# Kernel tuning notes

Hardware: AMD Instinct MI355X
Metric: run time of the kernel (lower is better)

The kernel has to match this reference:

```python
import jax, jax.numpy as jnp
import numpy as np

B, L, DK, DV, H = 2, 2048, 512, 512, 8
DH_K = DK // H  # 64
DH_V = DV // H  # 64


def setup_inputs() -> dict:
    key = jax.random.key(0)
    ks = jax.random.split(key, 6)
    scale_w = 1.0 / np.sqrt(DK)
    return {
        "keys": jax.random.normal(ks[0], (B, L, DK), dtype=jnp.float32),
        "queries": jax.random.normal(ks[1], (B, L, DK), dtype=jnp.float32),
        "values": jax.random.normal(ks[2], (B, L, DV), dtype=jnp.float32),
        "WQ": jax.random.normal(ks[3], (H, DK, DH_K), dtype=jnp.float32) * scale_w,
        "WK": jax.random.normal(ks[4], (H, DK, DH_K), dtype=jnp.float32) * scale_w,
        "WV": jax.random.normal(ks[5], (H, DV, DH_V), dtype=jnp.float32) * scale_w,
    }


def reference(keys, queries, values, WQ, WK, WV):
    # Per-head projections, vectorized over all H heads at once.
    Q = jnp.einsum('bld,hde->bhle', queries, WQ)   # [B,H,Lq,dh]
    K = jnp.einsum('bld,hde->bhle', keys, WK)      # [B,H,Lk,dh]
    V = jnp.einsum('bld,hde->bhle', values, WV)    # [B,H,Lk,dv_h]
    Lk = keys.shape[1]
    # NOTE: original scales by sqrt(seq_len_k), not sqrt(head_dim).
    y = jnp.einsum('bhqe,bhke->bhqk', Q, K) / jnp.sqrt(jnp.float32(Lk))
    # NOTE: original applies softmax over torch dim=1 of [B,Lq,Lk],
    # i.e. the QUERY axis (axis=2 here in [B,H,Lq,Lk]).
    z = jax.nn.softmax(y, axis=2)
    out = jnp.einsum('bhqk,bhke->bhqe', z, V)      # [B,H,Lq,dv_h]
    # Concat heads on the feature dim (same order as torch.concat(..., 2)).
    Bq, Hh, Lq, Dh = out.shape
    return out.transpose(0, 2, 1, 3).reshape(Bq, Lq, Hh * Dh)
```

## Files before the change

kernel.cpp:

```cpp
#include <hip/hip_runtime.h>
#include <hip/hip_bf16.h>

#define LL 2048
#define DM 512
#define SCALE 0.02209708691207961f

typedef unsigned short u16;
typedef __attribute__((ext_vector_type(8))) short short8;
typedef __attribute__((ext_vector_type(4))) short short4v;
typedef __attribute__((ext_vector_type(4))) float f32x4;

#define XAQ_OFF 0u
#define XAK_OFF 2097152u
#define WB_OFF  4194304u
#define QB_OFF  4980736u
#define KB_OFF  7077888u
#define VT_OFF  9175040u
#define SV_OFF  11272192u

__device__ __forceinline__ u16 f2bf(float f) {
  union { float f; unsigned u; } v; v.f = f;
  unsigned r = v.u + 0x7fff + ((v.u >> 16) & 1);
  return (u16)(r >> 16);
}
__device__ __forceinline__ float bf2f(u16 u) {
  union { unsigned u; float f; } v; v.u = ((unsigned)u) << 16; return v.f;
}

__global__ __launch_bounds__(256) void prep_kernel(
    const float* __restrict__ queries, const float* __restrict__ keys,
    const float* __restrict__ WQ, const float* __restrict__ WK,
    const float* __restrict__ WV, u16* __restrict__ wsb) {
  int t = threadIdx.x;
  if (blockIdx.x < 2048) {
    size_t c = (size_t)blockIdx.x * 256 + t;
    int tens = (int)(c >> 18);
    size_t off = (c & 262143u) * 8;
    int b  = (int)(off >> 20);
    int l  = (int)((off >> 9) & 2047);
    int d8 = (int)((off & 511) >> 3);
    int kt = d8 >> 2, quad = d8 & 3;
    const float* src = (tens ? keys : queries) + off;
    float4 a = *(const float4*)(src);
    float4 bb = *(const float4*)(src + 4);
    short8 o;
    o[0] = (short)f2bf(a.x); o[1] = (short)f2bf(a.y);
    o[2] = (short)f2bf(a.z); o[3] = (short)f2bf(a.w);
    o[4] = (short)f2bf(bb.x); o[5] = (short)f2bf(bb.y);
    o[6] = (short)f2bf(bb.z); o[7] = (short)f2bf(bb.w);
    size_t dst = (tens ? XAK_OFF : XAQ_OFF) +
        ((((size_t)b * 128 + (l >> 4)) * 16 + kt) * 64 + (quad * 16 + (l & 15))) * 8;
    *(short8*)(wsb + dst) = o;
  } else {
    int c2 = (blockIdx.x - 2048) * 256 + t;
    int lane = c2 & 63;
    int nt = (c2 >> 6) & 3;
    int kt = (c2 >> 8) & 15;
    int h  = (c2 >> 12) & 7;
    int z  = c2 >> 15;
    int quad = lane >> 4, l16 = lane & 15;
    const float* W = (z == 0) ? WQ : (z == 1) ? WK : WV;
    const float* src = W + ((size_t)h * DM + kt * 32 + quad * 8) * 64 + nt * 16 + l16;
    short8 o;
#pragma unroll
    for (int j = 0; j < 8; ++j) o[j] = (short)f2bf(src[(size_t)j * 64]);
    *(short8*)(wsb + WB_OFF + (size_t)c2 * 8) = o;
  }
}

__global__ __launch_bounds__(256) void proj_kernel(const float* __restrict__ values,
                                                   u16* __restrict__ wsb) {
  int t = threadIdx.x;
  int lane = t & 63, w = t >> 6, quad = lane >> 4, l16 = lane & 15;
  int z = blockIdx.z, bh = blockIdx.y, b = bh >> 3, h = bh & 7;
  int qbase = blockIdx.x * 64;

  const u16* Bw = wsb + WB_OFF + ((size_t)(z * 8 + h) * 16) * 4 * 64 * 8;

  __shared__ __align__(16) short As[64 * 40];

  f32x4 acc[4];
#pragma unroll
  for (int nt = 0; nt < 4; ++nt) acc[nt] = (f32x4){0.f, 0.f, 0.f, 0.f};

  if (z < 2) {
    const u16* Ab = wsb + ((z == 0) ? XAQ_OFF : XAK_OFF) +
        (((size_t)b * 128 + (qbase >> 4) + w) * 16) * 64 * 8;
#pragma unroll 4
    for (int kt = 0; kt < 16; ++kt) {
      short8 a = *(const short8*)(Ab + ((size_t)kt * 64 + lane) * 8);
#pragma unroll
      for (int nt = 0; nt < 4; ++nt) {
        short8 bb = *(const short8*)(Bw + (((size_t)kt * 4 + nt) * 64 + lane) * 8);
        acc[nt] = __builtin_amdgcn_mfma_f32_16x16x32_bf16(a, bb, acc[nt], 0, 0, 0);
      }
    }
  } else {
    const float* inbase = values + ((size_t)b * LL + qbase) * DM;
    for (int kt = 0; kt < 16; ++kt) {
      __syncthreads();
#pragma unroll
      for (int rep = 0; rep < 2; ++rep) {
        int f4 = t + rep * 256;
        int row = f4 >> 3, c4 = f4 & 7;
        float4 v = *(const float4*)(inbase + (size_t)row * DM + kt * 32 + c4 * 4);
        short* dst = &As[row * 40 + c4 * 4];
        dst[0] = (short)f2bf(v.x); dst[1] = (short)f2bf(v.y);
        dst[2] = (short)f2bf(v.z); dst[3] = (short)f2bf(v.w);
      }
      __syncthreads();
      short8 a = *(const short8*)&As[(w * 16 + l16) * 40 + quad * 8];
#pragma unroll
      for (int nt = 0; nt < 4; ++nt) {
        short8 bb = *(const short8*)(Bw + (((size_t)kt * 4 + nt) * 64 + lane) * 8);
        acc[nt] = __builtin_amdgcn_mfma_f32_16x16x32_bf16(a, bb, acc[nt], 0, 0, 0);
      }
    }
  }

  if (z == 0) {
    u16* og = wsb + QB_OFF + ((size_t)bh * LL + qbase) * 64;
#pragma unroll
    for (int nt = 0; nt < 4; ++nt)
#pragma unroll
      for (int r = 0; r < 4; ++r)
        og[(size_t)(w * 16 + quad * 4 + r) * 64 + nt * 16 + l16] = f2bf(acc[nt][r] * SCALE);
  } else if (z == 1) {
    u16* og = wsb + KB_OFF + ((size_t)bh * LL + qbase) * 64;
#pragma unroll
    for (int nt = 0; nt < 4; ++nt)
#pragma unroll
      for (int r = 0; r < 4; ++r)
        og[(size_t)(w * 16 + quad * 4 + r) * 64 + nt * 16 + l16] = f2bf(acc[nt][r]);
  } else {
    u16* og = wsb + VT_OFF + (size_t)bh * 64 * LL;
#pragma unroll
    for (int nt = 0; nt < 4; ++nt)
#pragma unroll
      for (int r = 0; r < 4; ++r)
        og[(size_t)(nt * 16 + l16) * LL + qbase + w * 16 + quad * 4 + r] = f2bf(acc[nt][r]);
  }
}

__global__ __launch_bounds__(256) void stats_kernel(u16* __restrict__ wsb,
                                                    float* __restrict__ Sinv) {
  const u16* Qb = wsb + QB_OFF;
  const u16* Kb = wsb + KB_OFF;
  int t = threadIdx.x;
  int lane = t & 63, w = t >> 6, quad = lane >> 4, l16 = lane & 15;
  int bh = blockIdx.y;
  int kbase = blockIdx.x * 64;

  short8 ka0 = *(const short8*)(Kb + ((size_t)bh * LL + kbase + w * 16 + l16) * 64 + quad * 8);
  short8 ka1 = *(const short8*)(Kb + ((size_t)bh * LL + kbase + w * 16 + l16) * 64 + quad * 8 + 32);

  __shared__ __align__(16) u16 Qsh[64 * 72];
  __shared__ float Ss[64];

  int srow = t >> 3, sc8 = t & 7;
  int srow2 = (t + 256) >> 3;

  const u16* Qg = Qb + (size_t)bh * LL * 64;
  short8 rq0 = *(const short8*)(Qg + (size_t)srow * 64 + sc8 * 8);
  short8 rq1 = *(const short8*)(Qg + (size_t)srow2 * 64 + sc8 * 8);

  float rs[4] = {0.f, 0.f, 0.f, 0.f};
  for (int qt = 0; qt < 32; ++qt) {
    __syncthreads();
    *(short8*)&Qsh[srow * 72 + sc8 * 8] = rq0;
    *(short8*)&Qsh[srow2 * 72 + sc8 * 8] = rq1;
    rq0 = *(const short8*)(Qg + (size_t)((qt + 1) * 64 + srow) * 64 + sc8 * 8);
    rq1 = *(const short8*)(Qg + (size_t)((qt + 1) * 64 + srow2) * 64 + sc8 * 8);
    __syncthreads();
#pragma unroll
    for (int nt = 0; nt < 4; ++nt) {
      short8 b0 = *(const short8*)&Qsh[(nt * 16 + l16) * 72 + quad * 8];
      short8 b1 = *(const short8*)&Qsh[(nt * 16 + l16) * 72 + quad * 8 + 32];
      f32x4 y = (f32x4){0.f, 0.f, 0.f, 0.f};
      y = __builtin_amdgcn_mfma_f32_16x16x32_bf16(ka0, b0, y, 0, 0, 0);
      y = __builtin_amdgcn_mfma_f32_16x16x32_bf16(ka1, b1, y, 0, 0, 0);
#pragma unroll
      for (int r = 0; r < 4; ++r) rs[r] += __expf(y[r]);
    }
  }
#pragma unroll
  for (int r = 0; r < 4; ++r) {
    rs[r] += __shfl_xor(rs[r], 1);
    rs[r] += __shfl_xor(rs[r], 2);
    rs[r] += __shfl_xor(rs[r], 4);
    rs[r] += __shfl_xor(rs[r], 8);
  }
  if (l16 == 0) {
#pragma unroll
    for (int r = 0; r < 4; ++r) {
      float s = 1.0f / rs[r];
      Sinv[(size_t)bh * LL + kbase + w * 16 + quad * 4 + r] = s;
      Ss[w * 16 + quad * 4 + r] = s;
    }
  }
  __syncthreads();
#pragma unroll
  for (int rep = 0; rep < 2; ++rep) {
    int f8 = t + rep * 256;
    int e = f8 >> 3, c8 = f8 & 7;
    size_t ad = VT_OFF + ((size_t)bh * 64 + e) * LL + kbase + c8 * 8;
    short8 v = *(const short8*)(wsb + ad);
#pragma unroll
    for (int i = 0; i < 8; ++i)
      v[i] = (short)f2bf(bf2f((u16)v[i]) * Ss[c8 * 8 + i]);
    *(short8*)(wsb + ad) = v;
  }
}

__global__ __launch_bounds__(256) void attn_kernel(const u16* __restrict__ wsb,
                                                   float* __restrict__ out) {
  const u16* Qb = wsb + QB_OFF;
  const u16* Kb = wsb + KB_OFF;
  const u16* Vt = wsb + VT_OFF;
  int t = threadIdx.x;
  int lane = t & 63, w = t >> 6, quad = lane >> 4, l16 = lane & 15;
  int bh = blockIdx.y, b = bh >> 3, h = bh & 7;
  int qbase = blockIdx.x * 64;

  __shared__ __align__(16) u16 Ksh[64 * 72];
  __shared__ __align__(16) u16 Vsh[64 * 72];
  __shared__ __align__(16) u16 Ps[4 * 16 * 72];
  u16* psw = Ps + w * 16 * 72;

  short8 qa0 = *(const short8*)(Qb + ((size_t)bh * LL + qbase + w * 16 + l16) * 64 + quad * 8);
  short8 qa1 = *(const short8*)(Qb + ((size_t)bh * LL + qbase + w * 16 + l16) * 64 + quad * 8 + 32);

  int srow = t >> 3, sc8 = t & 7;
  int srow2 = (t + 256) >> 3;
  const u16* Kg = Kb + (size_t)bh * LL * 64;
  const u16* Vg = Vt + (size_t)bh * 64 * LL;

  short8 rk0 = *(const short8*)(Kg + (size_t)srow * 64 + sc8 * 8);
  short8 rk1 = *(const short8*)(Kg + (size_t)srow2 * 64 + sc8 * 8);
  short8 rv0 = *(const short8*)(Vg + (size_t)srow * LL + sc8 * 8);
  short8 rv1 = *(const short8*)(Vg + (size_t)srow2 * LL + sc8 * 8);

  f32x4 oacc[4];
#pragma unroll
  for (int nt = 0; nt < 4; ++nt) oacc[nt] = (f32x4){0.f, 0.f, 0.f, 0.f};

  for (int kt = 0; kt < 32; ++kt) {
    __syncthreads();
    *(short8*)&Ksh[srow * 72 + sc8 * 8] = rk0;
    *(short8*)&Ksh[srow2 * 72 + sc8 * 8] = rk1;
    *(short8*)&Vsh[srow * 72 + sc8 * 8] = rv0;
    *(short8*)&Vsh[srow2 * 72 + sc8 * 8] = rv1;
    rk0 = *(const short8*)(Kg + (size_t)((kt + 1) * 64 + srow) * 64 + sc8 * 8);
    rk1 = *(const short8*)(Kg + (size_t)((kt + 1) * 64 + srow2) * 64 + sc8 * 8);
    rv0 = *(const short8*)(Vg + (size_t)srow * LL + (kt + 1) * 64 + sc8 * 8);
    rv1 = *(const short8*)(Vg + (size_t)srow2 * LL + (kt + 1) * 64 + sc8 * 8);
    __syncthreads();

#pragma unroll
    for (int mt = 0; mt < 4; ++mt) {
      short8 a0 = *(const short8*)&Ksh[(mt * 16 + l16) * 72 + quad * 8];
      short8 a1 = *(const short8*)&Ksh[(mt * 16 + l16) * 72 + quad * 8 + 32];
      f32x4 y = (f32x4){0.f, 0.f, 0.f, 0.f};
      y = __builtin_amdgcn_mfma_f32_16x16x32_bf16(a0, qa0, y, 0, 0, 0);
      y = __builtin_amdgcn_mfma_f32_16x16x32_bf16(a1, qa1, y, 0, 0, 0);
      short4v p;
      p[0] = (short)f2bf(__expf(y[0]));
      p[1] = (short)f2bf(__expf(y[1]));
      p[2] = (short)f2bf(__expf(y[2]));
      p[3] = (short)f2bf(__expf(y[3]));
      *(short4v*)&psw[l16 * 72 + mt * 16 + quad * 4] = p;
    }
    short8 pa0 = *(const short8*)&psw[l16 * 72 + quad * 8];
    short8 pa1 = *(const short8*)&psw[l16 * 72 + quad * 8 + 32];
#pragma unroll
    for (int nt = 0; nt < 4; ++nt) {
      short8 v0 = *(const short8*)&Vsh[(nt * 16 + l16) * 72 + quad * 8];
      short8 v1 = *(const short8*)&Vsh[(nt * 16 + l16) * 72 + quad * 8 + 32];
      oacc[nt] = __builtin_amdgcn_mfma_f32_16x16x32_bf16(pa0, v0, oacc[nt], 0, 0, 0);
      oacc[nt] = __builtin_amdgcn_mfma_f32_16x16x32_bf16(pa1, v1, oacc[nt], 0, 0, 0);
    }
  }

  float* og = out + ((size_t)b * LL + qbase) * 512 + h * 64;
#pragma unroll
  for (int nt = 0; nt < 4; ++nt)
#pragma unroll
    for (int r = 0; r < 4; ++r)
      og[(size_t)(w * 16 + quad * 4 + r) * 512 + nt * 16 + l16] = oacc[nt][r];
}

extern "C" void kernel_launch(void* const* d_in, const int* in_sizes, int n_in,
                              void* d_out, int out_size, void* d_ws, size_t ws_size,
                              hipStream_t stream) {
  const float* keys    = (const float*)d_in[0];
  const float* queries = (const float*)d_in[1];
  const float* values  = (const float*)d_in[2];
  const float* WQ      = (const float*)d_in[3];
  const float* WK      = (const float*)d_in[4];
  const float* WV      = (const float*)d_in[5];
  float* out = (float*)d_out;
  u16* wsb = (u16*)d_ws;
  float* Sinv = (float*)(wsb + SV_OFF);

  prep_kernel<<<dim3(2048 + 384), 256, 0, stream>>>(queries, keys, WQ, WK, WV, wsb);
  proj_kernel<<<dim3(32, 16, 3), 256, 0, stream>>>(values, wsb);
  stats_kernel<<<dim3(32, 16), 256, 0, stream>>>(wsb, Sinv);
  attn_kernel<<<dim3(32, 16), 256, 0, stream>>>(wsb, out);
}
```

Baseline: 157.3 us.

## Store Q/K/V in MFMA fragment order and drop LDS staging in attention

The projection now writes Q and K directly in MFMA operand-fragment order. The stats kernel writes scaled V in a fragment layout suited to the 16x16x16 MFMA. The attention kernel loads operands straight from global memory without LDS tiles or barriers in the main loop. Each wave handles a slice of the key dimension for all 64 queries, and the partial outputs are reduced through shared memory at the end. This removes per-iteration syncthreads and the LDS round-trip for P, but adds more accumulator registers (launch bounds of 2), a large LDS reduction buffer and an extra final reduction.

New measurement: 147.5 us. 1.07x faster.

```diff
diff --git a/kernel.cpp b/kernel.cpp
--- a/kernel.cpp
+++ b/kernel.cpp
@@ -13,10 +13,10 @@
 #define XAQ_OFF 0u
 #define XAK_OFF 2097152u
 #define WB_OFF  4194304u
-#define QB_OFF  4980736u
-#define KB_OFF  7077888u
+#define QA_OFF  4980736u
+#define KA_OFF  7077888u
 #define VT_OFF  9175040u
-#define SV_OFF  11272192u
+#define VB_OFF  11272192u
 
 __device__ __forceinline__ u16 f2bf(float f) {
   union { float f; unsigned u; } v; v.f = f;
@@ -25,6 +25,12 @@
 }
 __device__ __forceinline__ float bf2f(u16 u) {
   union { unsigned u; float f; } v; v.u = ((unsigned)u) << 16; return v.f;
+}
+__device__ __forceinline__ size_t frag_idx(int bh, int t64, int w, int c, int lane) {
+  return ((((size_t)(bh * 32 + t64) * 4 + w) * 2 + c) * 64 + lane) * 8;
+}
+__device__ __forceinline__ size_t vb_idx(int bh, int kt, int w, int et, int lane) {
+  return ((((size_t)(bh * 32 + kt) * 4 + w) * 4 + et) * 64 + lane) * 4;
 }
 
 __global__ __launch_bounds__(256) void prep_kernel(
@@ -73,10 +79,9 @@
   int t = threadIdx.x;
   int lane = t & 63, w = t >> 6, quad = lane >> 4, l16 = lane & 15;
   int z = blockIdx.z, bh = blockIdx.y, b = bh >> 3, h = bh & 7;
-  int qbase = blockIdx.x * 64;
+  int QT = blockIdx.x, qbase = QT * 64;
 
   const u16* Bw = wsb + WB_OFF + ((size_t)(z * 8 + h) * 16) * 4 * 64 * 8;
-
   __shared__ __align__(16) short As[64 * 40];
 
   f32x4 acc[4];
@@ -118,20 +123,20 @@
     }
   }
 
-  if (z == 0) {
-    u16* og = wsb + QB_OFF + ((size_t)bh * LL + qbase) * 64;
-#pragma unroll
-    for (int nt = 0; nt < 4; ++nt)
-#pragma unroll
-      for (int r = 0; r < 4; ++r)
-        og[(size_t)(w * 16 + quad * 4 + r) * 64 + nt * 16 + l16] = f2bf(acc[nt][r] * SCALE);
-  } else if (z == 1) {
-    u16* og = wsb + KB_OFF + ((size_t)bh * LL + qbase) * 64;
-#pragma unroll
-    for (int nt = 0; nt < 4; ++nt)
-#pragma unroll
-      for (int r = 0; r < 4; ++r)
-        og[(size_t)(w * 16 + quad * 4 + r) * 64 + nt * 16 + l16] = f2bf(acc[nt][r]);
+  if (z < 2) {
+    u16* base = wsb + ((z == 0) ? QA_OFF : KA_OFF);
+    float sc = (z == 0) ? SCALE : 1.0f;
+#pragma unroll
+    for (int nt = 0; nt < 4; ++nt) {
+      int c = nt >> 1;
+      int quadp = (nt & 1) * 2 + (l16 >> 3);
+      int j = l16 & 7;
+#pragma unroll
+      for (int r = 0; r < 4; ++r) {
+        int lanep = quadp * 16 + quad * 4 + r;
+        base[frag_idx(bh, QT, w, c, lanep) + j] = f2bf(acc[nt][r] * sc);
+      }
+    }
   } else {
     u16* og = wsb + VT_OFF + (size_t)bh * 64 * LL;
 #pragma unroll
@@ -142,151 +147,139 @@
   }
 }
 
-__global__ __launch_bounds__(256) void stats_kernel(u16* __restrict__ wsb,
-                                                    float* __restrict__ Sinv) {
-  const u16* Qb = wsb + QB_OFF;
-  const u16* Kb = wsb + KB_OFF;
+__global__ __launch_bounds__(256) void stats_kernel(u16* __restrict__ wsb) {
   int t = threadIdx.x;
   int lane = t & 63, w = t >> 6, quad = lane >> 4, l16 = lane & 15;
   int bh = blockIdx.y;
-  int kbase = blockIdx.x * 64;
-
-  short8 ka0 = *(const short8*)(Kb + ((size_t)bh * LL + kbase + w * 16 + l16) * 64 + quad * 8);
-  short8 ka1 = *(const short8*)(Kb + ((size_t)bh * LL + kbase + w * 16 + l16) * 64 + quad * 8 + 32);
-
-  __shared__ __align__(16) u16 Qsh[64 * 72];
+  int KT = blockIdx.x;
+
+  short8 ka[4][2];
+#pragma unroll
+  for (int mt = 0; mt < 4; ++mt)
+#pragma unroll
+    for (int c = 0; c < 2; ++c)
+      ka[mt][c] = *(const short8*)(wsb + KA_OFF + frag_idx(bh, KT, mt, c, lane));
+
+  float rs[4][4];
+#pragma unroll
+  for (int mt = 0; mt < 4; ++mt)
+#pragma unroll
+    for (int r = 0; r < 4; ++r) rs[mt][r] = 0.f;
+
+  for (int qt = 0; qt < 32; ++qt) {
+    short8 qb0 = *(const short8*)(wsb + QA_OFF + frag_idx(bh, qt, w, 0, lane));
+    short8 qb1 = *(const short8*)(wsb + QA_OFF + frag_idx(bh, qt, w, 1, lane));
+#pragma unroll
+    for (int mt = 0; mt < 4; ++mt) {
+      f32x4 y = (f32x4){0.f, 0.f, 0.f, 0.f};
+      y = __builtin_amdgcn_mfma_f32_16x16x32_bf16(ka[mt][0], qb0, y, 0, 0, 0);
+      y = __builtin_amdgcn_mfma_f32_16x16x32_bf16(ka[mt][1], qb1, y, 0, 0, 0);
+#pragma unroll
+      for (int r = 0; r < 4; ++r) rs[mt][r] += __expf(y[r]);
+    }
+  }
+#pragma unroll
+  for (int mt = 0; mt < 4; ++mt)
+#pragma unroll
+    for (int r = 0; r < 4; ++r) {
+      rs[mt][r] += __shfl_xor(rs[mt][r], 1);
+      rs[mt][r] += __shfl_xor(rs[mt][r], 2);
+      rs[mt][r] += __shfl_xor(rs[mt][r], 4);
+      rs[mt][r] += __shfl_xor(rs[mt][r], 8);
+    }
+
+  __shared__ float Sred[4][64];
   __shared__ float Ss[64];
-
-  int srow = t >> 3, sc8 = t & 7;
-  int srow2 = (t + 256) >> 3;
-
-  const u16* Qg = Qb + (size_t)bh * LL * 64;
-  short8 rq0 = *(const short8*)(Qg + (size_t)srow * 64 + sc8 * 8);
-  short8 rq1 = *(const short8*)(Qg + (size_t)srow2 * 64 + sc8 * 8);
-
-  float rs[4] = {0.f, 0.f, 0.f, 0.f};
-  for (int qt = 0; qt < 32; ++qt) {
-    __syncthreads();
-    *(short8*)&Qsh[srow * 72 + sc8 * 8] = rq0;
-    *(short8*)&Qsh[srow2 * 72 + sc8 * 8] = rq1;
-    rq0 = *(const short8*)(Qg + (size_t)((qt + 1) * 64 + srow) * 64 + sc8 * 8);
-    rq1 = *(const short8*)(Qg + (size_t)((qt + 1) * 64 + srow2) * 64 + sc8 * 8);
-    __syncthreads();
-#pragma unroll
-    for (int nt = 0; nt < 4; ++nt) {
-      short8 b0 = *(const short8*)&Qsh[(nt * 16 + l16) * 72 + quad * 8];
-      short8 b1 = *(const short8*)&Qsh[(nt * 16 + l16) * 72 + quad * 8 + 32];
-      f32x4 y = (f32x4){0.f, 0.f, 0.f, 0.f};
-      y = __builtin_amdgcn_mfma_f32_16x16x32_bf16(ka0, b0, y, 0, 0, 0);
-      y = __builtin_amdgcn_mfma_f32_16x16x32_bf16(ka1, b1, y, 0, 0, 0);
-#pragma unroll
-      for (int r = 0; r < 4; ++r) rs[r] += __expf(y[r]);
-    }
-  }
-#pragma unroll
-  for (int r = 0; r < 4; ++r) {
-    rs[r] += __shfl_xor(rs[r], 1);
-    rs[r] += __shfl_xor(rs[r], 2);
-    rs[r] += __shfl_xor(rs[r], 4);
-    rs[r] += __shfl_xor(rs[r], 8);
-  }
   if (l16 == 0) {
 #pragma unroll
-    for (int r = 0; r < 4; ++r) {
-      float s = 1.0f / rs[r];
-      Sinv[(size_t)bh * LL + kbase + w * 16 + quad * 4 + r] = s;
-      Ss[w * 16 + quad * 4 + r] = s;
-    }
+    for (int mt = 0; mt < 4; ++mt)
+#pragma unroll
+      for (int r = 0; r < 4; ++r)
+        Sred[w][mt * 16 + quad * 4 + r] = rs[mt][r];
   }
   __syncthreads();
+  if (t < 64) Ss[t] = 1.0f / (Sred[0][t] + Sred[1][t] + Sred[2][t] + Sred[3][t]);
+  __syncthreads();
+
 #pragma unroll
   for (int rep = 0; rep < 2; ++rep) {
     int f8 = t + rep * 256;
     int e = f8 >> 3, c8 = f8 & 7;
-    size_t ad = VT_OFF + ((size_t)bh * 64 + e) * LL + kbase + c8 * 8;
-    short8 v = *(const short8*)(wsb + ad);
-#pragma unroll
-    for (int i = 0; i < 8; ++i)
-      v[i] = (short)f2bf(bf2f((u16)v[i]) * Ss[c8 * 8 + i]);
-    *(short8*)(wsb + ad) = v;
-  }
-}
-
-__global__ __launch_bounds__(256) void attn_kernel(const u16* __restrict__ wsb,
-                                                   float* __restrict__ out) {
-  const u16* Qb = wsb + QB_OFF;
-  const u16* Kb = wsb + KB_OFF;
-  const u16* Vt = wsb + VT_OFF;
+    const u16* src = wsb + VT_OFF + ((size_t)bh * 64 + e) * LL + KT * 64 + c8 * 8;
+    short8 v = *(const short8*)src;
+    float sv[8];
+#pragma unroll
+    for (int i = 0; i < 8; ++i) sv[i] = bf2f((u16)v[i]) * Ss[c8 * 8 + i];
+    int wv = c8 >> 1, et = e >> 4;
+#pragma unroll
+    for (int g = 0; g < 2; ++g) {
+      short4v o;
+#pragma unroll
+      for (int j = 0; j < 4; ++j) o[j] = (short)f2bf(sv[g * 4 + j]);
+      int lanep = ((c8 & 1) * 2 + g) * 16 + (e & 15);
+      *(short4v*)(wsb + VB_OFF + vb_idx(bh, KT, wv, et, lanep)) = o;
+    }
+  }
+}
+
+__global__ __launch_bounds__(256, 2) void attn_kernel(const u16* __restrict__ wsb,
+                                                      float* __restrict__ out) {
   int t = threadIdx.x;
   int lane = t & 63, w = t >> 6, quad = lane >> 4, l16 = lane & 15;
   int bh = blockIdx.y, b = bh >> 3, h = bh & 7;
-  int qbase = blockIdx.x * 64;
-
-  __shared__ __align__(16) u16 Ksh[64 * 72];
-  __shared__ __align__(16) u16 Vsh[64 * 72];
-  __shared__ __align__(16) u16 Ps[4 * 16 * 72];
-  u16* psw = Ps + w * 16 * 72;
-
-  short8 qa0 = *(const short8*)(Qb + ((size_t)bh * LL + qbase + w * 16 + l16) * 64 + quad * 8);
-  short8 qa1 = *(const short8*)(Qb + ((size_t)bh * LL + qbase + w * 16 + l16) * 64 + quad * 8 + 32);
-
-  int srow = t >> 3, sc8 = t & 7;
-  int srow2 = (t + 256) >> 3;
-  const u16* Kg = Kb + (size_t)bh * LL * 64;
-  const u16* Vg = Vt + (size_t)bh * 64 * LL;
-
-  short8 rk0 = *(const short8*)(Kg + (size_t)srow * 64 + sc8 * 8);
-  short8 rk1 = *(const short8*)(Kg + (size_t)srow2 * 64 + sc8 * 8);
-  short8 rv0 = *(const short8*)(Vg + (size_t)srow * LL + sc8 * 8);
-  short8 rv1 = *(const short8*)(Vg + (size_t)srow2 * LL + sc8 * 8);
-
-  f32x4 oacc[4];
-#pragma unroll
-  for (int nt = 0; nt < 4; ++nt) oacc[nt] = (f32x4){0.f, 0.f, 0.f, 0.f};
+  int QT = blockIdx.x, qbase = QT * 64;
+
+  short8 qf[4][2];
+#pragma unroll
+  for (int nt = 0; nt < 4; ++nt)
+#pragma unroll
+    for (int c = 0; c < 2; ++c)
+      qf[nt][c] = *(const short8*)(wsb + QA_OFF + frag_idx(bh, QT, nt, c, lane));
+
+  f32x4 oacc[4][4];
+#pragma unroll
+  for (int nt = 0; nt < 4; ++nt)
+#pragma unroll
+    for (int et = 0; et < 4; ++et) oacc[nt][et] = (f32x4){0.f, 0.f, 0.f, 0.f};
 
   for (int kt = 0; kt < 32; ++kt) {
-    __syncthreads();
-    *(short8*)&Ksh[srow * 72 + sc8 * 8] = rk0;
-    *(short8*)&Ksh[srow2 * 72 + sc8 * 8] = rk1;
-    *(short8*)&Vsh[srow * 72 + sc8 * 8] = rv0;
-    *(short8*)&Vsh[srow2 * 72 + sc8 * 8] = rv1;
-    rk0 = *(const short8*)(Kg + (size_t)((kt + 1) * 64 + srow) * 64 + sc8 * 8);
-    rk1 = *(const short8*)(Kg + (size_t)((kt + 1) * 64 + srow2) * 64 + sc8 * 8);
-    rv0 = *(const short8*)(Vg + (size_t)srow * LL + (kt + 1) * 64 + sc8 * 8);
-    rv1 = *(const short8*)(Vg + (size_t)srow2 * LL + (kt + 1) * 64 + sc8 * 8);
-    __syncthreads();
-
-#pragma unroll
-    for (int mt = 0; mt < 4; ++mt) {
-      short8 a0 = *(const short8*)&Ksh[(mt * 16 + l16) * 72 + quad * 8];
-      short8 a1 = *(const short8*)&Ksh[(mt * 16 + l16) * 72 + quad * 8 + 32];
+    short8 ka0 = *(const short8*)(wsb + KA_OFF + frag_idx(bh, kt, w, 0, lane));
+    short8 ka1 = *(const short8*)(wsb + KA_OFF + frag_idx(bh, kt, w, 1, lane));
+    short4v vb[4];
+#pragma unroll
+    for (int et = 0; et < 4; ++et)
+      vb[et] = *(const short4v*)(wsb + VB_OFF + vb_idx(bh, kt, w, et, lane));
+
+#pragma unroll
+    for (int nt = 0; nt < 4; ++nt) {
       f32x4 y = (f32x4){0.f, 0.f, 0.f, 0.f};
-      y = __builtin_amdgcn_mfma_f32_16x16x32_bf16(a0, qa0, y, 0, 0, 0);
-      y = __builtin_amdgcn_mfma_f32_16x16x32_bf16(a1, qa1, y, 0, 0, 0);
-      short4v p;
-      p[0] = (short)f2bf(__expf(y[0]));
-      p[1] = (short)f2bf(__expf(y[1]));
-      p[2] = (short)f2bf(__expf(y[2]));
-      p[3] = (short)f2bf(__expf(y[3]));
-      *(short4v*)&psw[l16 * 72 + mt * 16 + quad * 4] = p;
-    }
-    short8 pa0 = *(const short8*)&psw[l16 * 72 + quad * 8];
-    short8 pa1 = *(const short8*)&psw[l16 * 72 + quad * 8 + 32];
-#pragma unroll
-    for (int nt = 0; nt < 4; ++nt) {
-      short8 v0 = *(const short8*)&Vsh[(nt * 16 + l16) * 72 + quad * 8];
-      short8 v1 = *(const short8*)&Vsh[(nt * 16 + l16) * 72 + quad * 8 + 32];
-      oacc[nt] = __builtin_amdgcn_mfma_f32_16x16x32_bf16(pa0, v0, oacc[nt], 0, 0, 0);
-      oacc[nt] = __builtin_amdgcn_mfma_f32_16x16x32_bf16(pa1, v1, oacc[nt], 0, 0, 0);
-    }
-  }
-
-  float* og = out + ((size_t)b * LL + qbase) * 512 + h * 64;
+      y = __builtin_amdgcn_mfma_f32_16x16x32_bf16(ka0, qf[nt][0], y, 0, 0, 0);
+      y = __builtin_amdgcn_mfma_f32_16x16x32_bf16(ka1, qf[nt][1], y, 0, 0, 0);
+      short4v pa;
+#pragma unroll
+      for (int r = 0; r < 4; ++r) pa[r] = (short)f2bf(__expf(y[r]));
+#pragma unroll
+      for (int et = 0; et < 4; ++et)
+        oacc[nt][et] = __builtin_amdgcn_mfma_f32_16x16x16bf16_1k(pa, vb[et], oacc[nt][et], 0, 0, 0);
+    }
+  }
+
+  __shared__ float red[4][64][68];
 #pragma unroll
   for (int nt = 0; nt < 4; ++nt)
 #pragma unroll
-    for (int r = 0; r < 4; ++r)
-      og[(size_t)(w * 16 + quad * 4 + r) * 512 + nt * 16 + l16] = oacc[nt][r];
+    for (int et = 0; et < 4; ++et)
+#pragma unroll
+      for (int r = 0; r < 4; ++r)
+        red[w][nt * 16 + quad * 4 + r][et * 16 + l16] = oacc[nt][et][r];
+  __syncthreads();
+  float* og = out + ((size_t)b * LL + qbase + w * 16) * 512 + h * 64;
+#pragma unroll
+  for (int i = 0; i < 16; ++i) {
+    float s = red[0][w * 16 + i][lane] + red[1][w * 16 + i][lane] +
+              red[2][w * 16 + i][lane] + red[3][w * 16 + i][lane];
+    og[(size_t)i * 512 + lane] = s;
+  }
 }
 
 extern "C" void kernel_launch(void* const* d_in, const int* in_sizes, int n_in,
@@ -300,10 +293,9 @@
   const float* WV      = (const float*)d_in[5];
   float* out = (float*)d_out;
   u16* wsb = (u16*)d_ws;
-  float* Sinv = (float*)(wsb + SV_OFF);
 
   prep_kernel<<<dim3(2048 + 384), 256, 0, stream>>>(queries, keys, WQ, WK, WV, wsb);
   proj_kernel<<<dim3(32, 16, 3), 256, 0, stream>>>(values, wsb);
-  stats_kernel<<<dim3(32, 16), 256, 0, stream>>>(wsb, Sinv);
+  stats_kernel<<<dim3(32, 16), 256, 0, stream>>>(wsb);
   attn_kernel<<<dim3(32, 16), 256, 0, stream>>>(wsb, out);
 }
```
